# Kernel tuning notes

Measured on AMD Instinct MI355X. Metric: run time of the kernel, lower is better.

The kernel has to match this reference:

```python
import jax, jax.numpy as jnp
import numpy as np

N_NODES = 100000
N_EDGES = 1600000
N_REL = 2
IN_CH, HID_CH, OUT_CH = 128, 128, 64


def setup_inputs() -> dict:
    key = jax.random.key(0)
    ks = jax.random.split(key, 8)
    x = jax.random.normal(ks[0], (N_NODES, IN_CH), dtype=jnp.float32)
    edge_index = jax.random.randint(ks[1], (2, N_EDGES), 0, N_NODES, dtype=jnp.int64)
    edge_type = jax.random.randint(ks[2], (N_EDGES,), 0, N_REL, dtype=jnp.int64)
    s1 = 1.0 / np.sqrt(IN_CH)
    s2 = 1.0 / np.sqrt(HID_CH)
    W1_rel = jax.random.normal(ks[3], (N_REL, IN_CH, HID_CH), dtype=jnp.float32) * s1
    W1_root = jax.random.normal(ks[4], (IN_CH, HID_CH), dtype=jnp.float32) * s1
    b1 = jnp.zeros((HID_CH,), dtype=jnp.float32)
    W2_rel = jax.random.normal(ks[5], (N_REL, HID_CH, OUT_CH), dtype=jnp.float32) * s2
    W2_root = jax.random.normal(ks[6], (HID_CH, OUT_CH), dtype=jnp.float32) * s2
    b2 = jnp.zeros((OUT_CH,), dtype=jnp.float32)
    return {"x": x, "edge_index": edge_index, "edge_type": edge_type,
            "W1_rel": W1_rel, "W1_root": W1_root, "b1": b1,
            "W2_rel": W2_rel, "W2_root": W2_root, "b2": b2}


def rgcn_conv(x, edge_index, edge_type, W_rel, W_root, b):
    """Relational graph conv: root transform + per-relation gather/matmul/scatter-mean."""
    src, dst = edge_index[0], edge_index[1]
    N = x.shape[0]
    out = x @ W_root + b  # self/root term
    x_src = x[src]  # [E, in] gather once, reused across relations
    for r in range(W_rel.shape[0]):  # N_REL is small and fixed
        mask = (edge_type == r)
        msg = jnp.where(mask[:, None], x_src, 0.0) @ W_rel[r]  # [E, out]
        agg = jax.ops.segment_sum(msg, dst, num_segments=N)  # [N, out]
        cnt = jax.ops.segment_sum(mask.astype(x.dtype), dst, num_segments=N)
        out = out + agg / jnp.maximum(cnt, 1.0)[:, None]  # mean aggregation
    return out


def l2_normalize(x, eps=1e-12):
    nrm = jnp.sqrt(jnp.sum(x * x, axis=1, keepdims=True))
    return x / jnp.maximum(nrm, eps)


def reference(x, edge_index, edge_type, W1_rel, W1_root, b1, W2_rel, W2_root, b2):
    h = jax.nn.relu(rgcn_conv(x, edge_index, edge_type, W1_rel, W1_root, b1))
    out = rgcn_conv(h, edge_index, edge_type, W2_rel, W2_root, b2)
    return l2_normalize(out)
```

## Files before the change

### kernel.cpp

```cpp
#include <hip/hip_runtime.h>
#include <hip/hip_bf16.h>


typedef unsigned int uint;
typedef unsigned short ushort;
typedef __attribute__((ext_vector_type(8))) short short8;
typedef __attribute__((ext_vector_type(16))) float floatx16;
typedef __attribute__((ext_vector_type(2))) float f32x2;
typedef __attribute__((ext_vector_type(4))) float f32x4;
typedef __attribute__((ext_vector_type(4))) uint u32x4;

#define IN_CH  128
#define OUT_CH 64
#define SCAN_CHUNK 2048
#define EPB 8192
#define KPB 512
#define MAXBK 400

__device__ __forceinline__ ushort f2bf(float f) {
    uint u = __float_as_uint(f);
    u += 0x7FFF + ((u >> 16) & 1);
    return (ushort)(u >> 16);
}
__device__ __forceinline__ float bflo(uint u) { return __uint_as_float(u << 16); }
__device__ __forceinline__ float bfhi(uint u) { return __uint_as_float(u & 0xFFFF0000u); }


__global__ void k_count(const int* __restrict__ dst, const int* __restrict__ et,
                        int* __restrict__ cntblk, int E, int NBK, int NBLK) {
    __shared__ int cnt[MAXBK];
    int tid = threadIdx.x, blk = blockIdx.x;
    for (int b = tid; b < NBK; b += 256) cnt[b] = 0;
    __syncthreads();
    int base = blk * EPB;
#pragma unroll 4
    for (int i = 0; i < EPB / 256; i++) {
        int e = base + i * 256 + tid;
        if (e < E) {
            int key = 2 * dst[e] + et[e];
            atomicAdd(&cnt[key >> 9], 1);
        }
    }
    __syncthreads();
    for (int b = tid; b < NBK; b += 256) cntblk[b * NBLK + blk] = cnt[b];
}

__global__ void k_scan_a(const int* __restrict__ deg, int* __restrict__ offs,
                         int* __restrict__ bsums, int n) {
    __shared__ int sdata[256];
    int b = blockIdx.x, t = threadIdx.x;
    int base = b * SCAN_CHUNK + t * 8;
    int v[8];
    int sum = 0;
#pragma unroll
    for (int i = 0; i < 8; i++) {
        int idx = base + i;
        int x = (idx < n) ? deg[idx] : 0;
        v[i] = sum;
        sum += x;
    }
    sdata[t] = sum;
    __syncthreads();
    for (int ofs = 1; ofs < 256; ofs <<= 1) {
        int val = sdata[t];
        int add = (t >= ofs) ? sdata[t - ofs] : 0;
        __syncthreads();
        sdata[t] = val + add;
        __syncthreads();
    }
    int texcl = (t == 0) ? 0 : sdata[t - 1];
    if (t == 255) bsums[b] = sdata[255];
#pragma unroll
    for (int i = 0; i < 8; i++) {
        int idx = base + i;
        if (idx < n) offs[idx] = texcl + v[i];
    }
}

__global__ void k_scan_b(int* __restrict__ bsums, int* __restrict__ offs, int nb, int n) {
    int t = threadIdx.x;
    if (nb <= 64) {
        int v = (t < nb) ? bsums[t] : 0;
        int s = v;
#pragma unroll
        for (int d = 1; d < 64; d <<= 1) {
            int u = __shfl_up(s, d, 64);
            if (t >= d) s += u;
        }
        if (t < nb) bsums[t] = s - v;
        if (t == 63) offs[n] = s;
    } else if (t == 0) {
        int run = 0;
        for (int b = 0; b < nb; b++) {
            int x = bsums[b];
            bsums[b] = run;
            run += x;
        }
        offs[n] = run;
    }
}

__global__ void k_part(const int* __restrict__ src, const int* __restrict__ dst,
                       const int* __restrict__ et, const int* __restrict__ basebb,
                       const int* __restrict__ bsums,
                       uint* __restrict__ stage, int E, int NBK, int NBLK) {
    __shared__ int cnt[MAXBK];
    __shared__ int basel[MAXBK];
    int tid = threadIdx.x, blk = blockIdx.x;
    for (int b = tid; b < NBK; b += 256) {
        cnt[b] = 0;
        int i = b * NBLK + blk;
        basel[b] = basebb[i] + bsums[i >> 11];
    }
    __syncthreads();
    int base = blk * EPB;
#pragma unroll 4
    for (int i = 0; i < EPB / 256; i++) {
        int e = base + i * 256 + tid;
        if (e < E) {
            int s = src[e];
            int key = 2 * dst[e] + et[e];
            int bk = key >> 9;
            int r = atomicAdd(&cnt[bk], 1);
            stage[basel[bk] + r] = ((uint)(key & 511) << 23) | (uint)s;
        }
    }
}

__global__ void k_fine(const uint* __restrict__ stage, const int* __restrict__ basebb,
                       const int* __restrict__ bsums,
                       int* __restrict__ offs, int* __restrict__ esrc,
                       int E, int NBK, int NBLK) {
    __shared__ int kcnt[KPB];
    __shared__ int kcur[KPB];
    __shared__ int ssum[256];
    int tid = threadIdx.x, b = blockIdx.x;
    int i0 = b * NBLK;
    int start = basebb[i0] + bsums[i0 >> 11];
    int endB = E;
    if (b != NBK - 1) {
        int i1 = (b + 1) * NBLK;
        endB = basebb[i1] + bsums[i1 >> 11];
    }
    int size = endB - start;

    kcnt[tid] = 0;
    kcnt[tid + 256] = 0;
    __syncthreads();
    for (int i = tid; i < size; i += 256)
        atomicAdd(&kcnt[stage[start + i] >> 23], 1);
    __syncthreads();
    int v0 = kcnt[2 * tid], v1 = kcnt[2 * tid + 1];
    ssum[tid] = v0 + v1;
    __syncthreads();
    for (int ofs = 1; ofs < 256; ofs <<= 1) {
        int val = ssum[tid];
        int add = (tid >= ofs) ? ssum[tid - ofs] : 0;
        __syncthreads();
        ssum[tid] = val + add;
        __syncthreads();
    }
    int texcl = (tid == 0) ? 0 : ssum[tid - 1];
    kcur[2 * tid] = texcl;
    kcur[2 * tid + 1] = texcl + v0;
    offs[(b << 9) + 2 * tid] = start + texcl + v0;
    offs[(b << 9) + 2 * tid + 1] = start + texcl + v0 + v1;
    __syncthreads();
    for (int i = tid; i < size; i += 256) {
        uint p = stage[start + i];
        int r = atomicAdd(&kcur[p >> 23], 1);
        esrc[start + r] = (int)(p & 0x7FFFFFu);
    }
}


__device__ __forceinline__ uint4 pack8(const ushort* o) {
    uint4 v;
    v.x = (uint)o[0] | ((uint)o[1] << 16);
    v.y = (uint)o[2] | ((uint)o[3] << 16);
    v.z = (uint)o[4] | ((uint)o[5] << 16);
    v.w = (uint)o[6] | ((uint)o[7] << 16);
    return v;
}

__global__ void k_cvtprep(const float* __restrict__ x, uint4* __restrict__ xb, int n8,
                          const float* __restrict__ W1root, const float* __restrict__ W1rel,
                          const float* __restrict__ W2root, const float* __restrict__ W2rel,
                          uint4* __restrict__ Bpk1, uint4* __restrict__ Bpk2,
                          uint* __restrict__ xzero, uint* __restrict__ t2zero) {
    int bid = blockIdx.x, tid = threadIdx.x;
    if (bid < 40) {
        if (bid == 0) {
            if (tid < 64) xzero[tid] = 0;
            if (tid < 96) t2zero[tid] = 0;
        }
        int idx = bid * 256 + tid;
        ushort o[8];
        if (idx < 6144) {
            int id = idx;
            int ct = id >> 11;
            int c = id & 2047;
            int gn = c >> 9, s = (c >> 6) & 7, h = (c >> 5) & 1, n = c & 31;
            int k0 = s * 16 + h * 8;
            int col = gn * 32 + n;
            const float* W = (ct == 0) ? W1root : (W1rel + (size_t)(ct - 1) * 16384);
#pragma unroll
            for (int j = 0; j < 8; j++) o[j] = f2bf(W[(k0 + j) * 128 + col]);
            Bpk1[id] = pack8(o);
        } else {
            int id = idx - 6144;
            int ct = id >> 11;
            int c = id & 2047;
            int gn = c >> 9, s = (c >> 6) & 7, h = (c >> 5) & 1, n = c & 31;
            int k0 = s * 16 + h * 8;
            int colg = ct * 128 + gn * 32 + n;
#pragma unroll
            for (int j = 0; j < 8; j++) {
                float f = 0.f;
                if (colg < 64)       f = W2root[(k0 + j) * 64 + colg];
                else if (colg < 128) f = W2rel[(k0 + j) * 64 + (colg - 64)];
                else if (colg < 192) f = W2rel[8192 + (k0 + j) * 64 + (colg - 128)];
                o[j] = f2bf(f);
            }
            Bpk2[id] = pack8(o);
        }
    } else {
        int i = (bid - 40) * 256 + tid;
        if (i >= n8) return;
        const f32x4* xp = (const f32x4*)x;
        f32x4 f0 = __builtin_nontemporal_load(&xp[(size_t)i * 2]);
        f32x4 f1 = __builtin_nontemporal_load(&xp[(size_t)i * 2 + 1]);
        uint4 o;
        o.x = (uint)f2bf(f0.x) | ((uint)f2bf(f0.y) << 16);
        o.y = (uint)f2bf(f0.z) | ((uint)f2bf(f0.w) << 16);
        o.z = (uint)f2bf(f1.x) | ((uint)f2bf(f1.y) << 16);
        o.w = (uint)f2bf(f1.z) | ((uint)f2bf(f1.w) << 16);
        xb[i] = o;
    }
}


__global__ __launch_bounds__(256)
void k_agg(const int* __restrict__ offs, const int* __restrict__ esrc,
           const uint4* __restrict__ xb4, uint* __restrict__ S, int N) {
    int wid = (int)((blockIdx.x * 256L + threadIdx.x) >> 5);
    int l = threadIdx.x & 31;
    if (wid >= N) return;
    int q = l >> 4, c = l & 15;

    int beg0 = (wid == 0) ? 0 : offs[2 * wid - 1];
    int end0 = offs[2 * wid], end1 = offs[2 * wid + 1];

    u32x4 o = {0, 0, 0, 0};
#pragma unroll
    for (int r = 0; r < 2; r++) {
        int beg = r ? end0 : beg0;
        int end = r ? end1 : end0;
        f32x2 a0 = {0.f, 0.f}, a1 = {0.f, 0.f}, a2 = {0.f, 0.f}, a3 = {0.f, 0.f};
        for (int c0 = beg; c0 < end; c0 += 32) {
            int myid = (c0 + l < end) ? __builtin_nontemporal_load(&esrc[c0 + l]) : N;
            int m = min(32, end - c0);
            for (int eb = 0; eb < m; eb += 4) {
#pragma unroll
                for (int j = 0; j < 2; j++) {
                    int id = __shfl(myid, eb + 2 * j + q, 32);
                    uint4 v = xb4[(uint)id * 16u + (uint)c];
                    a0 += (f32x2){bflo(v.x), bfhi(v.x)};
                    a1 += (f32x2){bflo(v.y), bfhi(v.y)};
                    a2 += (f32x2){bflo(v.z), bfhi(v.z)};
                    a3 += (f32x2){bflo(v.w), bfhi(v.w)};
                }
            }
        }
        a0.x += __shfl_xor(a0.x, 16, 32); a0.y += __shfl_xor(a0.y, 16, 32);
        a1.x += __shfl_xor(a1.x, 16, 32); a1.y += __shfl_xor(a1.y, 16, 32);
        a2.x += __shfl_xor(a2.x, 16, 32); a2.y += __shfl_xor(a2.y, 16, 32);
        a3.x += __shfl_xor(a3.x, 16, 32); a3.y += __shfl_xor(a3.y, 16, 32);
        if (q == r) {
            float inv = (end > beg) ? 1.0f / (float)(end - beg) : 0.f;
            o.x = (uint)f2bf(a0.x * inv) | ((uint)f2bf(a0.y * inv) << 16);
            o.y = (uint)f2bf(a1.x * inv) | ((uint)f2bf(a1.y * inv) << 16);
            o.z = (uint)f2bf(a2.x * inv) | ((uint)f2bf(a2.y * inv) << 16);
            o.w = (uint)f2bf(a3.x * inv) | ((uint)f2bf(a3.y * inv) << 16);
        }
    }
    u32x4* Sp = (u32x4*)S;
    __builtin_nontemporal_store(o, &Sp[(size_t)wid * 32 + q * 16 + c]);
}


__global__ __launch_bounds__(256)
void k_gemm1(const ushort* __restrict__ xb, const ushort* __restrict__ S1,
             const ushort* __restrict__ Bpk, const float* __restrict__ b1,
             ushort* __restrict__ h, int N) {
    __shared__ ushort SH[32768];
    ushort* Alds = SH;
    ushort* Blds = SH + 16384;

    const int tid = threadIdx.x;
    const int lane = tid & 63;
    const int w = tid >> 6;
    const int wm = w >> 1, wn = w & 1;
    const int rowBase = blockIdx.x * 128;

    floatx16 acc[2][2] = {};

#pragma unroll
    for (int seg = 0; seg < 3; seg++) {
        const ushort* Ap = (seg == 0) ? xb : S1;
        const int stride = (seg == 0) ? 128 : 256;
        const int aoff = (seg == 2) ? 128 : 0;
        const uint4* Bsrc = (const uint4*)Bpk + seg * 2048;
#pragma unroll
        for (int i = 0; i < 8; i++) {
            int c = tid + i * 256;
            int m = c & 31, hh = (c >> 5) & 1, s = (c >> 6) & 7, g = c >> 9;
            int row = rowBase + g * 32 + m;
            if (row >= N) row = N - 1;
            int kc = s * 2 + hh;
            ((uint4*)Alds)[c] = *(const uint4*)(Ap + (size_t)row * stride + aoff + kc * 8);
            ((uint4*)Blds)[c] = Bsrc[c];
        }
        __syncthreads();
#pragma unroll
        for (int s = 0; s < 8; s++) {
            short8 a0 = *(const short8*)&Alds[(((wm * 2 + 0) * 8 + s) * 64 + lane) * 8];
            short8 a1 = *(const short8*)&Alds[(((wm * 2 + 1) * 8 + s) * 64 + lane) * 8];
            short8 b0 = *(const short8*)&Blds[(((wn * 2 + 0) * 8 + s) * 64 + lane) * 8];
            short8 b1f = *(const short8*)&Blds[(((wn * 2 + 1) * 8 + s) * 64 + lane) * 8];
            acc[0][0] = __builtin_amdgcn_mfma_f32_32x32x16_bf16(a0, b0, acc[0][0], 0, 0, 0);
            acc[0][1] = __builtin_amdgcn_mfma_f32_32x32x16_bf16(a0, b1f, acc[0][1], 0, 0, 0);
            acc[1][0] = __builtin_amdgcn_mfma_f32_32x32x16_bf16(a1, b0, acc[1][0], 0, 0, 0);
            acc[1][1] = __builtin_amdgcn_mfma_f32_32x32x16_bf16(a1, b1f, acc[1][1], 0, 0, 0);
        }
        __syncthreads();
    }

    ushort* Clds = SH;
    const int qr = 4 * (lane >> 5);
    const int cl = lane & 31;
    float bb[2];
#pragma unroll
    for (int nt = 0; nt < 2; nt++) bb[nt] = b1[wn * 64 + nt * 32 + cl];
#pragma unroll
    for (int mt = 0; mt < 2; mt++)
#pragma unroll
        for (int nt = 0; nt < 2; nt++) {
#pragma unroll
            for (int reg = 0; reg < 16; reg++) {
                int rl = (reg & 3) + 8 * (reg >> 2) + qr;
                float v = fmaxf(acc[mt][nt][reg] + bb[nt], 0.f);
                Clds[(wm * 64 + mt * 32 + rl) * 136 + wn * 64 + nt * 32 + cl] = f2bf(v);
            }
        }
    __syncthreads();

    int r = tid >> 1, half = tid & 1;
    int grow = rowBase + r;
    if (grow < N) {
#pragma unroll
        for (int k = 0; k < 8; k++) {
            int c0 = half * 64 + k * 8;
            uint4 v = *(const uint4*)&Clds[r * 136 + c0];
            *(uint4*)(h + (size_t)grow * 128 + c0) = v;
        }
    }
}


__global__ __launch_bounds__(256)
void k_gemmT(const ushort* __restrict__ A, const ushort* __restrict__ Bpk,
             ushort* __restrict__ Out, int N) {
    __shared__ ushort SH[40960];
    ushort* Alds = SH;
    ushort* Blds = SH + 16384;

    const int tid = threadIdx.x;
    const int lane = tid & 63;
    const int w = tid >> 6;
    const int wm = w >> 1, wn = w & 1;
    const int rowBase = blockIdx.x * 128;

    const uint4* Bsrc = (const uint4*)Bpk;
#pragma unroll
    for (int i = 0; i < 12; i++) {
        int c = tid + i * 256;
        ((uint4*)Blds)[c] = Bsrc[c];
    }
#pragma unroll
    for (int i = 0; i < 8; i++) {
        int c = tid + i * 256;
        int m = c & 31, hh = (c >> 5) & 1, s = (c >> 6) & 7, g = c >> 9;
        int row = rowBase + g * 32 + m;
        if (row >= N) row = N - 1;
        int kc = s * 2 + hh;
        ((uint4*)Alds)[c] = *(const uint4*)(A + (size_t)row * 128 + kc * 8);
    }
    __syncthreads();

    floatx16 acc[2][3] = {};
#pragma unroll
    for (int s = 0; s < 8; s++) {
        short8 a0 = *(const short8*)&Alds[(((wm * 2 + 0) * 8 + s) * 64 + lane) * 8];
        short8 a1 = *(const short8*)&Alds[(((wm * 2 + 1) * 8 + s) * 64 + lane) * 8];
        short8 b0 = *(const short8*)&Blds[((wn * 3 + 0) * 512 + s * 64 + lane) * 8];
        short8 b1 = *(const short8*)&Blds[((wn * 3 + 1) * 512 + s * 64 + lane) * 8];
        short8 b2 = *(const short8*)&Blds[((wn * 3 + 2) * 512 + s * 64 + lane) * 8];
        acc[0][0] = __builtin_amdgcn_mfma_f32_32x32x16_bf16(a0, b0, acc[0][0], 0, 0, 0);
        acc[0][1] = __builtin_amdgcn_mfma_f32_32x32x16_bf16(a0, b1, acc[0][1], 0, 0, 0);
        acc[0][2] = __builtin_amdgcn_mfma_f32_32x32x16_bf16(a0, b2, acc[0][2], 0, 0, 0);
        acc[1][0] = __builtin_amdgcn_mfma_f32_32x32x16_bf16(a1, b0, acc[1][0], 0, 0, 0);
        acc[1][1] = __builtin_amdgcn_mfma_f32_32x32x16_bf16(a1, b1, acc[1][1], 0, 0, 0);
        acc[1][2] = __builtin_amdgcn_mfma_f32_32x32x16_bf16(a1, b2, acc[1][2], 0, 0, 0);
    }
    __syncthreads();

    ushort* Clds = SH;
    const int qr = 4 * (lane >> 5);
    const int cl = lane & 31;
#pragma unroll
    for (int mt = 0; mt < 2; mt++)
#pragma unroll
        for (int nt = 0; nt < 3; nt++) {
#pragma unroll
            for (int reg = 0; reg < 16; reg++) {
                int rl = (reg & 3) + 8 * (reg >> 2) + qr;
                Clds[(wm * 64 + mt * 32 + rl) * 200 + wn * 96 + nt * 32 + cl] =
                    f2bf(acc[mt][nt][reg]);
            }
        }
    __syncthreads();

    int r = tid >> 1, half = tid & 1;
    int grow = rowBase + r;
    if (grow < N) {
#pragma unroll
        for (int k = 0; k < 12; k++) {
            int c0 = half * 96 + k * 8;
            uint4 v = *(const uint4*)&Clds[r * 200 + c0];
            *(uint4*)(Out + (size_t)grow * 192 + c0) = v;
        }
    }
}


__global__ __launch_bounds__(256)
void k_final(const ushort* __restrict__ T2, const float* __restrict__ b2,
             const int* __restrict__ offs, const int* __restrict__ esrc,
             float* __restrict__ out, int N) {
    int wid = (int)((blockIdx.x * 256L + threadIdx.x) >> 3);
    int c = threadIdx.x & 7;
    if (wid >= N) return;
    const uint4* Tb = (const uint4*)T2;

    int beg0 = (wid == 0) ? 0 : offs[2 * wid - 1];
    int end0 = offs[2 * wid], end1 = offs[2 * wid + 1];

    f32x2 t0 = {0.f, 0.f}, t1 = {0.f, 0.f}, t2v = {0.f, 0.f}, t3v = {0.f, 0.f};
#pragma unroll
    for (int r = 0; r < 2; r++) {
        int beg = r ? end0 : beg0;
        int end = r ? end1 : end0;
        if (end > beg) {
            f32x2 a0 = {0.f, 0.f}, a1 = {0.f, 0.f}, a2 = {0.f, 0.f}, a3 = {0.f, 0.f};
            uint bc = 8u + 8u * (uint)r + (uint)c;
            for (int c0 = beg; c0 < end; c0 += 8) {
                int myid = (c0 + c < end) ? __builtin_nontemporal_load(&esrc[c0 + c]) : N;
                int m = min(8, end - c0);
                for (int eb = 0; eb < m; eb += 4) {
                    uint4 v[4];
#pragma unroll
                    for (int j = 0; j < 4; j++) {
                        int id = __shfl(myid, eb + j, 8);
                        v[j] = Tb[(uint)id * 24u + bc];
                    }
#pragma unroll
                    for (int j = 0; j < 4; j++) {
                        a0 += (f32x2){bflo(v[j].x), bfhi(v[j].x)};
                        a1 += (f32x2){bflo(v[j].y), bfhi(v[j].y)};
                        a2 += (f32x2){bflo(v[j].z), bfhi(v[j].z)};
                        a3 += (f32x2){bflo(v[j].w), bfhi(v[j].w)};
                    }
                }
            }
            float inv = 1.0f / (float)(end - beg);
            t0 += a0 * inv; t1 += a1 * inv; t2v += a2 * inv; t3v += a3 * inv;
        }
    }
    uint4 ru = Tb[(uint)wid * 24u + (uint)c];
    float4 bbA = *(const float4*)(b2 + 8 * c);
    float4 bbB = *(const float4*)(b2 + 8 * c + 4);
    float v0 = bflo(ru.x) + bbA.x + t0.x;
    float v1 = bfhi(ru.x) + bbA.y + t0.y;
    float v2 = bflo(ru.y) + bbA.z + t1.x;
    float v3 = bfhi(ru.y) + bbA.w + t1.y;
    float v4 = bflo(ru.z) + bbB.x + t2v.x;
    float v5 = bfhi(ru.z) + bbB.y + t2v.y;
    float v6 = bflo(ru.w) + bbB.z + t3v.x;
    float v7 = bfhi(ru.w) + bbB.w + t3v.y;
    float sq = v0 * v0 + v1 * v1 + v2 * v2 + v3 * v3
             + v4 * v4 + v5 * v5 + v6 * v6 + v7 * v7;
#pragma unroll
    for (int d = 1; d <= 4; d <<= 1) sq += __shfl_xor(sq, d, 8);
    float rn = 1.0f / fmaxf(sqrtf(sq), 1e-12f);
    f32x4 oA = {v0 * rn, v1 * rn, v2 * rn, v3 * rn};
    f32x4 oB = {v4 * rn, v5 * rn, v6 * rn, v7 * rn};
    f32x4* op = (f32x4*)(out + (size_t)wid * 64 + 8 * c);
    __builtin_nontemporal_store(oA, op);
    __builtin_nontemporal_store(oB, op + 1);
}


extern "C" void kernel_launch(void* const* d_in, const int* in_sizes, int n_in,
                              void* d_out, int out_size, void* d_ws, size_t ws_size,
                              hipStream_t stream) {
    const float* x      = (const float*)d_in[0];
    const int*   ei     = (const int*)d_in[1];
    const int*   etype  = (const int*)d_in[2];
    const float* W1rel  = (const float*)d_in[3];
    const float* W1root = (const float*)d_in[4];
    const float* b1     = (const float*)d_in[5];
    const float* W2rel  = (const float*)d_in[6];
    const float* W2root = (const float*)d_in[7];
    const float* b2     = (const float*)d_in[8];
    float* out = (float*)d_out;

    const int N = in_sizes[0] / IN_CH;
    const int E = in_sizes[2];
    const int NKEY = 2 * N;
    const int NBK  = (NKEY + KPB - 1) / KPB;
    const int NBLK = (E + EPB - 1) / EPB;
    const int NSC  = NBK * NBLK;

    const int* src = ei;
    const int* dst = ei + E;

    char* base = (char*)d_ws;
    size_t off = 0;
    auto carve = [&](size_t bytes) -> void* {
        void* p = base + off;
        off = (off + bytes + 511) & ~(size_t)511;
        return p;
    };
    ushort* xb    = (ushort*)carve((size_t)(N + 1) * 128 * sizeof(ushort));
    ushort* hA    = (ushort*)carve((size_t)N * 128 * sizeof(ushort));
    ushort* S1    = (ushort*)carve((size_t)N * 256 * sizeof(ushort));
    ushort* t2    = (ushort*)carve((size_t)(N + 1) * 192 * sizeof(ushort));
    int*    esrc  = (int*)carve((size_t)E * sizeof(int));
    uint*   stage = (uint*)carve((size_t)E * sizeof(uint));
    int*    offs  = (int*)carve((size_t)NBK * KPB * sizeof(int));
    int*    cntblk= (int*)carve((size_t)NSC * sizeof(int));
    int*    basebb= (int*)carve((size_t)(NSC + 1) * sizeof(int));
    int     NB    = (NSC + SCAN_CHUNK - 1) / SCAN_CHUNK;
    int*    bsums = (int*)carve((size_t)NB * sizeof(int));
    uint4*  Bpk1  = (uint4*)carve(6144 * sizeof(uint4));
    uint4*  Bpk2  = (uint4*)carve(4096 * sizeof(uint4));
    (void)ws_size; (void)n_in; (void)out_size;

    int n8 = N * 16;
    int cvtBlocks = 40 + (n8 + 255) / 256;

    k_cvtprep<<<cvtBlocks, 256, 0, stream>>>(x, (uint4*)xb, n8,
                                             W1root, W1rel, W2root, W2rel,
                                             Bpk1, Bpk2,
                                             (uint*)(xb + (size_t)N * 128),
                                             (uint*)(t2 + (size_t)N * 192));

    k_count<<<NBLK, 256, 0, stream>>>(dst, etype, cntblk, E, NBK, NBLK);
    k_scan_a<<<NB, 256, 0, stream>>>(cntblk, basebb, bsums, NSC);
    k_scan_b<<<1, 64, 0, stream>>>(bsums, basebb, NB, NSC);
    k_part<<<NBLK, 256, 0, stream>>>(src, dst, etype, basebb, bsums, stage, E, NBK, NBLK);
    k_fine<<<NBK, 256, 0, stream>>>(stage, basebb, bsums, offs, esrc, E, NBK, NBLK);

    int rowTiles = (N + 127) / 128;
    int aggBlocks = (N + 7) / 8;
    int finBlocks = (N + 31) / 32;

    k_agg<<<aggBlocks, 256, 0, stream>>>(offs, esrc, (const uint4*)xb, (uint*)S1, N);
    k_gemm1<<<rowTiles, 256, 0, stream>>>(xb, S1, (const ushort*)Bpk1, b1, hA, N);

    k_gemmT<<<rowTiles, 256, 0, stream>>>(hA, (const ushort*)Bpk2, t2, N);
    k_final<<<finBlocks, 256, 0, stream>>>(t2, b2, offs, esrc, out, N);
}
```

Before: 349.8 us.

## Fuse layer-1 GEMM with layer-2 transform GEMM and merge count with conversion kernel

Merges k_gemm1 and k_gemmT into a single kernel. The ReLU'd hidden tile is written straight into LDS in the MFMA A-operand layout and immediately multiplied by the packed layer-2 weights, so the bf16 hidden matrix never makes a round trip through global memory. Separately, the edge-count kernel is folded into the conversion/weight-packing kernel as extra blocks, which removes one launch and lets both run concurrently. The fused kernel uses more LDS (80KB) and more registers, which may lower occupancy.

```diff
diff --git a/kernel.cpp b/kernel.cpp
--- a/kernel.cpp
+++ b/kernel.cpp
@@ -25,25 +25,6 @@
 __device__ __forceinline__ float bflo(uint u) { return __uint_as_float(u << 16); }
 __device__ __forceinline__ float bfhi(uint u) { return __uint_as_float(u & 0xFFFF0000u); }
 
-
-__global__ void k_count(const int* __restrict__ dst, const int* __restrict__ et,
-                        int* __restrict__ cntblk, int E, int NBK, int NBLK) {
-    __shared__ int cnt[MAXBK];
-    int tid = threadIdx.x, blk = blockIdx.x;
-    for (int b = tid; b < NBK; b += 256) cnt[b] = 0;
-    __syncthreads();
-    int base = blk * EPB;
-#pragma unroll 4
-    for (int i = 0; i < EPB / 256; i++) {
-        int e = base + i * 256 + tid;
-        if (e < E) {
-            int key = 2 * dst[e] + et[e];
-            atomicAdd(&cnt[key >> 9], 1);
-        }
-    }
-    __syncthreads();
-    for (int b = tid; b < NBK; b += 256) cntblk[b * NBLK + blk] = cnt[b];
-}
 
 __global__ void k_scan_a(const int* __restrict__ deg, int* __restrict__ offs,
                          int* __restrict__ bsums, int n) {
@@ -183,12 +164,33 @@
     return v;
 }
 
-__global__ void k_cvtprep(const float* __restrict__ x, uint4* __restrict__ xb, int n8,
-                          const float* __restrict__ W1root, const float* __restrict__ W1rel,
-                          const float* __restrict__ W2root, const float* __restrict__ W2rel,
-                          uint4* __restrict__ Bpk1, uint4* __restrict__ Bpk2,
-                          uint* __restrict__ xzero, uint* __restrict__ t2zero) {
-    int bid = blockIdx.x, tid = threadIdx.x;
+__global__ void k_pre(const int* __restrict__ dst, const int* __restrict__ et,
+                      int* __restrict__ cntblk, int E, int NBK, int NBLK,
+                      const float* __restrict__ x, uint4* __restrict__ xb, int n8,
+                      const float* __restrict__ W1root, const float* __restrict__ W1rel,
+                      const float* __restrict__ W2root, const float* __restrict__ W2rel,
+                      uint4* __restrict__ Bpk1, uint4* __restrict__ Bpk2,
+                      uint* __restrict__ xzero, uint* __restrict__ t2zero) {
+    __shared__ int cnt[MAXBK];
+    int tid = threadIdx.x;
+    if ((int)blockIdx.x < NBLK) {
+        int blk = blockIdx.x;
+        for (int b = tid; b < NBK; b += 256) cnt[b] = 0;
+        __syncthreads();
+        int base = blk * EPB;
+#pragma unroll 4
+        for (int i = 0; i < EPB / 256; i++) {
+            int e = base + i * 256 + tid;
+            if (e < E) {
+                int key = 2 * dst[e] + et[e];
+                atomicAdd(&cnt[key >> 9], 1);
+            }
+        }
+        __syncthreads();
+        for (int b = tid; b < NBK; b += 256) cntblk[b * NBLK + blk] = cnt[b];
+        return;
+    }
+    int bid = blockIdx.x - NBLK;
     if (bid < 40) {
         if (bid == 0) {
             if (tid < 64) xzero[tid] = 0;
@@ -290,10 +292,10 @@
 
 
 __global__ __launch_bounds__(256)
-void k_gemm1(const ushort* __restrict__ xb, const ushort* __restrict__ S1,
-             const ushort* __restrict__ Bpk, const float* __restrict__ b1,
-             ushort* __restrict__ h, int N) {
-    __shared__ ushort SH[32768];
+void k_fused(const ushort* __restrict__ xb, const ushort* __restrict__ S1,
+             const ushort* __restrict__ Bpk1, const float* __restrict__ b1,
+             const ushort* __restrict__ Bpk2, ushort* __restrict__ Out, int N) {
+    __shared__ ushort SH[40960];
     ushort* Alds = SH;
     ushort* Blds = SH + 16384;
 
@@ -310,7 +312,7 @@
         const ushort* Ap = (seg == 0) ? xb : S1;
         const int stride = (seg == 0) ? 128 : 256;
         const int aoff = (seg == 2) ? 128 : 0;
-        const uint4* Bsrc = (const uint4*)Bpk + seg * 2048;
+        const uint4* Bsrc = (const uint4*)Bpk1 + seg * 2048;
 #pragma unroll
         for (int i = 0; i < 8; i++) {
             int c = tid + i * 256;
@@ -336,99 +338,71 @@
         __syncthreads();
     }
 
-    ushort* Clds = SH;
-    const int qr = 4 * (lane >> 5);
-    const int cl = lane & 31;
-    float bb[2];
-#pragma unroll
-    for (int nt = 0; nt < 2; nt++) bb[nt] = b1[wn * 64 + nt * 32 + cl];
-#pragma unroll
-    for (int mt = 0; mt < 2; mt++)
-#pragma unroll
-        for (int nt = 0; nt < 2; nt++) {
-#pragma unroll
-            for (int reg = 0; reg < 16; reg++) {
-                int rl = (reg & 3) + 8 * (reg >> 2) + qr;
-                float v = fmaxf(acc[mt][nt][reg] + bb[nt], 0.f);
-                Clds[(wm * 64 + mt * 32 + rl) * 136 + wn * 64 + nt * 32 + cl] = f2bf(v);
+    {
+        const int qr = 4 * (lane >> 5);
+        const int cl = lane & 31;
+        float bb[2];
+#pragma unroll
+        for (int nt = 0; nt < 2; nt++) bb[nt] = b1[wn * 64 + nt * 32 + cl];
+#pragma unroll
+        for (int mt = 0; mt < 2; mt++)
+#pragma unroll
+            for (int nt = 0; nt < 2; nt++) {
+                int col = wn * 64 + nt * 32 + cl;
+                int kc = col >> 3, j = col & 7;
+                int s = kc >> 1, hh = kc & 1;
+                int base = (((wm * 2 + mt) * 8 + s) * 64 + hh * 32) * 8 + j;
+#pragma unroll
+                for (int reg = 0; reg < 16; reg++) {
+                    int rl = (reg & 3) + 8 * (reg >> 2) + qr;
+                    float v = fmaxf(acc[mt][nt][reg] + bb[nt], 0.f);
+                    Alds[base + rl * 8] = f2bf(v);
+                }
             }
-        }
-    __syncthreads();
-
-    int r = tid >> 1, half = tid & 1;
-    int grow = rowBase + r;
-    if (grow < N) {
-#pragma unroll
-        for (int k = 0; k < 8; k++) {
-            int c0 = half * 64 + k * 8;
-            uint4 v = *(const uint4*)&Clds[r * 136 + c0];
-            *(uint4*)(h + (size_t)grow * 128 + c0) = v;
-        }
-    }
-}
-
-
-__global__ __launch_bounds__(256)
-void k_gemmT(const ushort* __restrict__ A, const ushort* __restrict__ Bpk,
-             ushort* __restrict__ Out, int N) {
-    __shared__ ushort SH[40960];
-    ushort* Alds = SH;
-    ushort* Blds = SH + 16384;
-
-    const int tid = threadIdx.x;
-    const int lane = tid & 63;
-    const int w = tid >> 6;
-    const int wm = w >> 1, wn = w & 1;
-    const int rowBase = blockIdx.x * 128;
-
-    const uint4* Bsrc = (const uint4*)Bpk;
-#pragma unroll
-    for (int i = 0; i < 12; i++) {
-        int c = tid + i * 256;
-        ((uint4*)Blds)[c] = Bsrc[c];
-    }
-#pragma unroll
-    for (int i = 0; i < 8; i++) {
-        int c = tid + i * 256;
-        int m = c & 31, hh = (c >> 5) & 1, s = (c >> 6) & 7, g = c >> 9;
-        int row = rowBase + g * 32 + m;
-        if (row >= N) row = N - 1;
-        int kc = s * 2 + hh;
-        ((uint4*)Alds)[c] = *(const uint4*)(A + (size_t)row * 128 + kc * 8);
-    }
-    __syncthreads();
-
-    floatx16 acc[2][3] = {};
+    }
+    {
+        const uint4* B2 = (const uint4*)Bpk2;
+#pragma unroll
+        for (int i = 0; i < 12; i++) {
+            int c = tid + i * 256;
+            ((uint4*)Blds)[c] = B2[c];
+        }
+    }
+    __syncthreads();
+
+    floatx16 acc2[2][3] = {};
 #pragma unroll
     for (int s = 0; s < 8; s++) {
         short8 a0 = *(const short8*)&Alds[(((wm * 2 + 0) * 8 + s) * 64 + lane) * 8];
         short8 a1 = *(const short8*)&Alds[(((wm * 2 + 1) * 8 + s) * 64 + lane) * 8];
         short8 b0 = *(const short8*)&Blds[((wn * 3 + 0) * 512 + s * 64 + lane) * 8];
-        short8 b1 = *(const short8*)&Blds[((wn * 3 + 1) * 512 + s * 64 + lane) * 8];
-        short8 b2 = *(const short8*)&Blds[((wn * 3 + 2) * 512 + s * 64 + lane) * 8];
-        acc[0][0] = __builtin_amdgcn_mfma_f32_32x32x16_bf16(a0, b0, acc[0][0], 0, 0, 0);
-        acc[0][1] = __builtin_amdgcn_mfma_f32_32x32x16_bf16(a0, b1, acc[0][1], 0, 0, 0);
-        acc[0][2] = __builtin_amdgcn_mfma_f32_32x32x16_bf16(a0, b2, acc[0][2], 0, 0, 0);
-        acc[1][0] = __builtin_amdgcn_mfma_f32_32x32x16_bf16(a1, b0, acc[1][0], 0, 0, 0);
-        acc[1][1] = __builtin_amdgcn_mfma_f32_32x32x16_bf16(a1, b1, acc[1][1], 0, 0, 0);
-        acc[1][2] = __builtin_amdgcn_mfma_f32_32x32x16_bf16(a1, b2, acc[1][2], 0, 0, 0);
+        short8 b1v = *(const short8*)&Blds[((wn * 3 + 1) * 512 + s * 64 + lane) * 8];
+        short8 b2v = *(const short8*)&Blds[((wn * 3 + 2) * 512 + s * 64 + lane) * 8];
+        acc2[0][0] = __builtin_amdgcn_mfma_f32_32x32x16_bf16(a0, b0, acc2[0][0], 0, 0, 0);
+        acc2[0][1] = __builtin_amdgcn_mfma_f32_32x32x16_bf16(a0, b1v, acc2[0][1], 0, 0, 0);
+        acc2[0][2] = __builtin_amdgcn_mfma_f32_32x32x16_bf16(a0, b2v, acc2[0][2], 0, 0, 0);
+        acc2[1][0] = __builtin_amdgcn_mfma_f32_32x32x16_bf16(a1, b0, acc2[1][0], 0, 0, 0);
+        acc2[1][1] = __builtin_amdgcn_mfma_f32_32x32x16_bf16(a1, b1v, acc2[1][1], 0, 0, 0);
+        acc2[1][2] = __builtin_amdgcn_mfma_f32_32x32x16_bf16(a1, b2v, acc2[1][2], 0, 0, 0);
     }
     __syncthreads();
 
     ushort* Clds = SH;
-    const int qr = 4 * (lane >> 5);
-    const int cl = lane & 31;
-#pragma unroll
-    for (int mt = 0; mt < 2; mt++)
-#pragma unroll
-        for (int nt = 0; nt < 3; nt++) {
-#pragma unroll
-            for (int reg = 0; reg < 16; reg++) {
-                int rl = (reg & 3) + 8 * (reg >> 2) + qr;
-                Clds[(wm * 64 + mt * 32 + rl) * 200 + wn * 96 + nt * 32 + cl] =
-                    f2bf(acc[mt][nt][reg]);
+    {
+        const int qr = 4 * (lane >> 5);
+        const int cl = lane & 31;
+#pragma unroll
+        for (int mt = 0; mt < 2; mt++)
+#pragma unroll
+            for (int nt = 0; nt < 3; nt++) {
+#pragma unroll
+                for (int reg = 0; reg < 16; reg++) {
+                    int rl = (reg & 3) + 8 * (reg >> 2) + qr;
+                    Clds[(wm * 64 + mt * 32 + rl) * 200 + wn * 96 + nt * 32 + cl] =
+                        f2bf(acc2[mt][nt][reg]);
+                }
             }
-        }
+    }
     __syncthreads();
 
     int r = tid >> 1, half = tid & 1;
@@ -543,7 +517,6 @@
         return p;
     };
     ushort* xb    = (ushort*)carve((size_t)(N + 1) * 128 * sizeof(ushort));
-    ushort* hA    = (ushort*)carve((size_t)N * 128 * sizeof(ushort));
     ushort* S1    = (ushort*)carve((size_t)N * 256 * sizeof(ushort));
     ushort* t2    = (ushort*)carve((size_t)(N + 1) * 192 * sizeof(ushort));
     int*    esrc  = (int*)carve((size_t)E * sizeof(int));
@@ -558,15 +531,15 @@
     (void)ws_size; (void)n_in; (void)out_size;
 
     int n8 = N * 16;
-    int cvtBlocks = 40 + (n8 + 255) / 256;
-
-    k_cvtprep<<<cvtBlocks, 256, 0, stream>>>(x, (uint4*)xb, n8,
-                                             W1root, W1rel, W2root, W2rel,
-                                             Bpk1, Bpk2,
-                                             (uint*)(xb + (size_t)N * 128),
-                                             (uint*)(t2 + (size_t)N * 192));
-
-    k_count<<<NBLK, 256, 0, stream>>>(dst, etype, cntblk, E, NBK, NBLK);
+    int preBlocks = NBLK + 40 + (n8 + 255) / 256;
+
+    k_pre<<<preBlocks, 256, 0, stream>>>(dst, etype, cntblk, E, NBK, NBLK,
+                                         x, (uint4*)xb, n8,
+                                         W1root, W1rel, W2root, W2rel,
+                                         Bpk1, Bpk2,
+                                         (uint*)(xb + (size_t)N * 128),
+                                         (uint*)(t2 + (size_t)N * 192));
+
     k_scan_a<<<NB, 256, 0, stream>>>(cntblk, basebb, bsums, NSC);
     k_scan_b<<<1, 64, 0, stream>>>(bsums, basebb, NB, NSC);
     k_part<<<NBLK, 256, 0, stream>>>(src, dst, etype, basebb, bsums, stage, E, NBK, NBLK);
@@ -577,8 +550,8 @@
     int finBlocks = (N + 31) / 32;
 
     k_agg<<<aggBlocks, 256, 0, stream>>>(offs, esrc, (const uint4*)xb, (uint*)S1, N);
-    k_gemm1<<<rowTiles, 256, 0, stream>>>(xb, S1, (const ushort*)Bpk1, b1, hA, N);
-
-    k_gemmT<<<rowTiles, 256, 0, stream>>>(hA, (const ushort*)Bpk2, t2, N);
+    k_fused<<<rowTiles, 256, 0, stream>>>(xb, S1, (const ushort*)Bpk1, b1,
+                                          (const ushort*)Bpk2, t2, N);
+
     k_final<<<finBlocks, 256, 0, stream>>>(t2, b2, offs, esrc, out, N);
 }
```

Result: faster. 330.9 us (-5.4%).
